# Optimization experiments

Measured on AMD Instinct MI355X. Metric: run time of the kernel, lower is better.

## Reference

```python
import jax, jax.numpy as jnp
import numpy as np

B, S, HID = 4, 1024, 768
H, D = 12, 32              # attention_head_size = (HID/H)//2
AH = H * D                 # all_head_size = 384
SCALING = D ** (-0.5)


def setup_inputs() -> dict:
    key = jax.random.key(0)
    ks = jax.random.split(key, 6)
    hidden_states = jax.random.normal(ks[0], (B, S, HID), dtype=jnp.float32)
    attention_mask = jnp.zeros((B, 1, 1, S), dtype=jnp.float32)
    init = 0.02
    Wq = jax.random.normal(ks[1], (AH, HID), dtype=jnp.float32) * init
    Wk1 = jax.random.normal(ks[2], (AH, HID), dtype=jnp.float32) * init
    Wk2 = jax.random.normal(ks[3], (AH, HID), dtype=jnp.float32) * init
    Wv = jax.random.normal(ks[4], (AH, HID), dtype=jnp.float32) * init
    bq = jnp.zeros((AH,), jnp.float32)
    bk1 = jnp.zeros((AH,), jnp.float32)
    bk2 = jnp.zeros((AH,), jnp.float32)
    bv = jnp.zeros((AH,), jnp.float32)
    pi = jnp.ones((2, H), jnp.float32) / 2.0
    return {"hidden_states": hidden_states, "attention_mask": attention_mask,
            "Wq": Wq, "bq": bq, "Wk1": Wk1, "bk1": bk1, "Wk2": Wk2, "bk2": bk2,
            "Wv": Wv, "bv": bv, "pi": pi}


def _heads(x):
    # [B,S,AH] -> [B,H,S,D]
    return x.reshape(B, S, H, D).transpose(0, 2, 1, 3)


def _sq_dist(x1, x2):
    # gpytorch Distance._sq_dist (postprocess=False): mean-adjust, then
    # ||x1||^2 + ||x2||^2 - 2 x1 x2^T, clamped at 0.
    adj = x1.mean(axis=-2, keepdims=True)
    x1 = x1 - adj
    x2 = x2 - adj
    n1 = (x1 * x1).sum(-1, keepdims=True)            # [B,H,S,1]
    n2 = (x2 * x2).sum(-1, keepdims=True)            # [B,H,S,1]
    cross = jnp.einsum('bhqd,bhkd->bhqk', x1, x2)    # [B,H,S,S]
    return jnp.maximum(n1 + jnp.swapaxes(n2, -1, -2) - 2.0 * cross, 0.0)


def reference(hidden_states, attention_mask, Wq, bq, Wk1, bk1, Wk2, bk2, Wv, bv, pi):
    q = _heads(hidden_states @ Wq.T + bq)
    k1 = _heads(hidden_states @ Wk1.T + bk1)
    k2 = _heads(hidden_states @ Wk2.T + bk2)
    v = _heads(hidden_states @ Wv.T + bv)

    d1 = -SCALING / 2.0 * _sq_dist(q, k1) + attention_mask
    d2 = -1.5 * SCALING / 2.0 * _sq_dist(q, k2) + attention_mask
    d1 = d1 - d1.max(axis=-1, keepdims=True)
    d2 = d2 - d2.max(axis=-1, keepdims=True)

    pi_c = jnp.clip(pi, 1e-6, 2.0)                   # clamp per original
    scores = (jnp.exp(d1) * pi_c[0][None, :, None, None]
              + jnp.exp(d2) * pi_c[1][None, :, None, None])
    probs = scores / (scores.sum(axis=-1, keepdims=True) + 1e-6)
    # dropout is identity in eval mode
    ctx = jnp.einsum('bhqk,bhkd->bhqd', probs, v)
    ctx = ctx.transpose(0, 2, 1, 3).reshape(B, S, AH)
    return (ctx, probs)
```

## Files before the change

### kernel.cpp

```cpp
#include <hip/hip_runtime.h>
#include <math.h>

#define BB 4
#define SS 1024
#define HH 12
#define DD 32
#define HIDDEN 768
#define AHS 384
#define RQ 8
#define HEAD_ELEMS (SS*DD)
#define CTX_ELEMS (BB*SS*AHS)

__device__ __forceinline__ float clampf(float x, float lo, float hi){ return fminf(fmaxf(x, lo), hi); }

__global__ __launch_bounds__(256)
void proj_kernel(const float* __restrict__ X,
                 const float* __restrict__ W0, const float* __restrict__ b0,
                 const float* __restrict__ W1, const float* __restrict__ b1,
                 const float* __restrict__ W2, const float* __restrict__ b2,
                 const float* __restrict__ W3, const float* __restrict__ b3,
                 float* __restrict__ qo, float* __restrict__ k1o,
                 float* __restrict__ k2o, float* __restrict__ vo)
{
    const int BM = 128, BN = 64, BK = 16;
    __shared__ float Xs[BK][BM + 4];
    __shared__ float Wsh[BK][BN + 4];
    int t  = threadIdx.x;
    int m0 = blockIdx.x * BM;
    int n0 = blockIdx.y * BN;
    int mat = n0 / AHS;
    int c0  = n0 % AHS;
    const float* W    = (mat==0) ? W0 : (mat==1) ? W1 : (mat==2) ? W2 : W3;
    const float* bias = (mat==0) ? b0 : (mat==1) ? b1 : (mat==2) ? b2 : b3;

    int tx = t & 15, ty = t >> 4;
    int lr = t >> 2;
    int lc = (t & 3) << 2;

    float acc[8][4];
    #pragma unroll
    for (int i = 0; i < 8; i++)
        #pragma unroll
        for (int j = 0; j < 4; j++) acc[i][j] = 0.f;

    float4 xa = *(const float4*)(X + (m0 + lr) * HIDDEN + lc);
    float4 xb = *(const float4*)(X + (m0 + 64 + lr) * HIDDEN + lc);
    float4 wa = *(const float4*)(W + (c0 + lr) * HIDDEN + lc);

    for (int k0 = 0; k0 < HIDDEN; k0 += BK) {
        __syncthreads();
        Xs[lc+0][lr] = xa.x; Xs[lc+1][lr] = xa.y; Xs[lc+2][lr] = xa.z; Xs[lc+3][lr] = xa.w;
        Xs[lc+0][64+lr] = xb.x; Xs[lc+1][64+lr] = xb.y; Xs[lc+2][64+lr] = xb.z; Xs[lc+3][64+lr] = xb.w;
        Wsh[lc+0][lr] = wa.x; Wsh[lc+1][lr] = wa.y; Wsh[lc+2][lr] = wa.z; Wsh[lc+3][lr] = wa.w;
        __syncthreads();
        if (k0 + BK < HIDDEN) {
            xa = *(const float4*)(X + (m0 + lr) * HIDDEN + k0 + BK + lc);
            xb = *(const float4*)(X + (m0 + 64 + lr) * HIDDEN + k0 + BK + lc);
            wa = *(const float4*)(W + (c0 + lr) * HIDDEN + k0 + BK + lc);
        }
        #pragma unroll
        for (int kk = 0; kk < BK; kk++) {
            float a[8], w4[4];
            *(float4*)&a[0] = *(const float4*)&Xs[kk][ty << 3];
            *(float4*)&a[4] = *(const float4*)&Xs[kk][(ty << 3) + 4];
            *(float4*)w4    = *(const float4*)&Wsh[kk][tx << 2];
            #pragma unroll
            for (int i = 0; i < 8; i++)
                #pragma unroll
                for (int j = 0; j < 4; j++)
                    acc[i][j] = fmaf(a[i], w4[j], acc[i][j]);
        }
    }

    int cbase = c0 + (tx << 2);
    int h  = (cbase >> 5) % HH;
    int d0 = cbase & 31;
    int d4 = d0 >> 2;
    float4 bq4 = *(const float4*)(bias + cbase);

    #pragma unroll
    for (int i = 0; i < 8; i++) {
        int row = m0 + (ty << 3) + i;
        int b_  = row >> 10;
        int s   = row & 1023;
        int bh  = b_ * HH + h;
        float4 val;
        val.x = acc[i][0] + bq4.x;
        val.y = acc[i][1] + bq4.y;
        val.z = acc[i][2] + bq4.z;
        val.w = acc[i][3] + bq4.w;
        if (mat == 0)
            *(float4*)&qo[((size_t)(bh * SS + s)) * DD + d0] = val;
        else if (mat == 1)
            *(float4*)&k1o[((size_t)(bh * 8 + d4) * SS + s) * 4] = val;
        else if (mat == 2)
            *(float4*)&k2o[((size_t)(bh * 8 + d4) * SS + s) * 4] = val;
        else
            *(float4*)&vo[((size_t)(bh * SS + s)) * DD + d0] = val;
    }
}

__global__ __launch_bounds__(256)
void norms_kernel(const float* __restrict__ k1i, const float* __restrict__ k2i,
                  float* __restrict__ n1, float* __restrict__ n2)
{
    int bh = blockIdx.y;
    int s  = blockIdx.x * 256 + threadIdx.x;
    const float* p1 = k1i + (size_t)bh * (8 * SS * 4) + s * 4;
    const float* p2 = k2i + (size_t)bh * (8 * SS * 4) + s * 4;
    float a1 = 0.f, a2 = 0.f;
    #pragma unroll
    for (int d4 = 0; d4 < 8; d4++) {
        float4 v1 = *(const float4*)&p1[(size_t)d4 * SS * 4];
        float4 v2 = *(const float4*)&p2[(size_t)d4 * SS * 4];
        a1 = fmaf(v1.x, v1.x, a1); a1 = fmaf(v1.y, v1.y, a1);
        a1 = fmaf(v1.z, v1.z, a1); a1 = fmaf(v1.w, v1.w, a1);
        a2 = fmaf(v2.x, v2.x, a2); a2 = fmaf(v2.y, v2.y, a2);
        a2 = fmaf(v2.z, v2.z, a2); a2 = fmaf(v2.w, v2.w, a2);
    }
    n1[bh * SS + s] = a1;
    n2[bh * SS + s] = a2;
}

__global__ __launch_bounds__(256, 4)
void attn_fused(const float* __restrict__ qg,  const float* __restrict__ k1i,
                const float* __restrict__ k2i,
                const float* __restrict__ n1g, const float* __restrict__ n2g,
                const float* __restrict__ maskg, const float* __restrict__ pig,
                const float* __restrict__ vg,
                float* __restrict__ probs, float* __restrict__ ctx)
{
    const float A1C = 0.08838834764831845f;
    const float A2C = 0.13258252147247767f;
    __shared__ float p_s[RQ * SS];
    __shared__ float q_s[RQ * DD];
    __shared__ float red1[4][RQ], red2[4][RQ];
    __shared__ float qn_s[RQ];

    int t    = threadIdx.x;
    int lane = t & 63, wid = t >> 6;

    int bid = blockIdx.x;
    int swz = (bid & 7) * 768 + (bid >> 3);
    int bh  = swz >> 7;
    int s0  = (swz & 127) * RQ;
    int b   = bh / HH, h = bh - b * HH;

    q_s[t] = qg[(bh * SS + s0) * DD + t];
    __syncthreads();
    if (t < RQ) {
        float a = 0.f;
        for (int d = 0; d < DD; d++) { float x = q_s[t * DD + d]; a = fmaf(x, x, a); }
        qn_s[t] = a;
    }
    __syncthreads();

    float pi0 = clampf(pig[h],      1e-6f, 2.0f);
    float pi1 = clampf(pig[HH + h], 1e-6f, 2.0f);

    float e1r[4][RQ], e2r[4][RQ];
    float pm1[RQ], pm2[RQ];
    #pragma unroll
    for (int r = 0; r < RQ; r++) { pm1[r] = -3.4e38f; pm2[r] = -3.4e38f; }

    const float* k1p = k1i + (size_t)bh * (8 * SS * 4);
    const float* k2p = k2i + (size_t)bh * (8 * SS * 4);
    const float* n1p = n1g + bh * SS;
    const float* n2p = n2g + bh * SS;
    const float* mp  = maskg + b * SS;

    #pragma unroll
    for (int j = 0; j < 4; j++) {
        int k = j * 256 + t;
        float n1k = n1p[k], n2k = n2p[k], mk = mp[k];
        float c1[RQ], c2[RQ];
        #pragma unroll
        for (int r = 0; r < RQ; r++) { c1[r] = 0.f; c2[r] = 0.f; }
        #pragma unroll
        for (int d4 = 0; d4 < 8; d4++) {
            float4 kq1 = *(const float4*)&k1p[((size_t)d4 * SS + k) * 4];
            float4 kq2 = *(const float4*)&k2p[((size_t)d4 * SS + k) * 4];
            const float* kv1 = (const float*)&kq1;
            const float* kv2 = (const float*)&kq2;
            #pragma unroll
            for (int r = 0; r < RQ; r++) {
                float qv[4];
                *(float4*)qv = *(const float4*)&q_s[r * DD + d4 * 4];
                #pragma unroll
                for (int dd = 0; dd < 4; dd++) {
                    c1[r] = fmaf(qv[dd], kv1[dd], c1[r]);
                    c2[r] = fmaf(qv[dd], kv2[dd], c2[r]);
                }
            }
        }
        #pragma unroll
        for (int r = 0; r < RQ; r++) {
            float qn  = qn_s[r];
            float d1v = fmaxf(fmaf(-2.f, c1[r], qn + n1k), 0.f);
            float d2v = fmaxf(fmaf(-2.f, c2[r], qn + n2k), 0.f);
            float ev1 = fmaf(-A1C, d1v, mk);
            float ev2 = fmaf(-A2C, d2v, mk);
            e1r[j][r] = ev1;
            e2r[j][r] = ev2;
            pm1[r] = fmaxf(pm1[r], ev1);
            pm2[r] = fmaxf(pm2[r], ev2);
        }
    }

    #pragma unroll
    for (int off = 32; off >= 1; off >>= 1)
        #pragma unroll
        for (int r = 0; r < RQ; r++) {
            pm1[r] = fmaxf(pm1[r], __shfl_xor(pm1[r], off));
            pm2[r] = fmaxf(pm2[r], __shfl_xor(pm2[r], off));
        }
    if (lane == 0) {
        #pragma unroll
        for (int r = 0; r < RQ; r++) { red1[wid][r] = pm1[r]; red2[wid][r] = pm2[r]; }
    }
    __syncthreads();
    float m1[RQ], m2[RQ];
    #pragma unroll
    for (int r = 0; r < RQ; r++) {
        m1[r] = fmaxf(fmaxf(red1[0][r], red1[1][r]), fmaxf(red1[2][r], red1[3][r]));
        m2[r] = fmaxf(fmaxf(red2[0][r], red2[1][r]), fmaxf(red2[2][r], red2[3][r]));
    }

    float ps[RQ];
    #pragma unroll
    for (int r = 0; r < RQ; r++) ps[r] = 0.f;
    #pragma unroll
    for (int j = 0; j < 4; j++)
        #pragma unroll
        for (int r = 0; r < RQ; r++) {
            float p = pi0 * __expf(e1r[j][r] - m1[r]) + pi1 * __expf(e2r[j][r] - m2[r]);
            e1r[j][r] = p;
            ps[r] += p;
        }

    #pragma unroll
    for (int off = 32; off >= 1; off >>= 1)
        #pragma unroll
        for (int r = 0; r < RQ; r++) ps[r] += __shfl_xor(ps[r], off);
    __syncthreads();
    if (lane == 0) {
        #pragma unroll
        for (int r = 0; r < RQ; r++) red1[wid][r] = ps[r];
    }
    __syncthreads();
    float inv[RQ];
    #pragma unroll
    for (int r = 0; r < RQ; r++) {
        float sum = red1[0][r] + red1[1][r] + red1[2][r] + red1[3][r];
        inv[r] = 1.0f / (sum + 1e-6f);
    }

    float* prow = probs + (size_t)(bh * SS + s0) * SS;
    #pragma unroll
    for (int j = 0; j < 4; j++) {
        int k = (j << 8) + t;
        float pv8[8];
        #pragma unroll
        for (int r = 0; r < RQ; r++) pv8[r] = e1r[j][r] * inv[r];
        #pragma unroll
        for (int r = 0; r < RQ; r++)
            __builtin_nontemporal_store(pv8[r], &prow[(size_t)r * SS + k]);
        int base = (k << 3) ^ (((k >> 5) & 3) << 3);
        *(float4*)&p_s[base]     = *(float4*)&pv8[0];
        *(float4*)&p_s[base + 4] = *(float4*)&pv8[4];
    }
    __syncthreads();

    {
        int ks = t >> 3;
        int c4 = t & 7;
        int swzc = (ks & 3) << 3;
        const float* vp = vg + bh * HEAD_ELEMS + (c4 << 2);
        float4 acc4[RQ];
        #pragma unroll
        for (int r = 0; r < RQ; r++) acc4[r] = make_float4(0.f, 0.f, 0.f, 0.f);
        #pragma unroll 4
        for (int kk = 0; kk < 32; kk++) {
            int k = (ks << 5) + kk;
            int base = (k << 3) ^ swzc;
            float pr[8];
            *(float4*)&pr[0] = *(const float4*)&p_s[base];
            *(float4*)&pr[4] = *(const float4*)&p_s[base + 4];
            float4 vv = *(const float4*)&vp[k << 5];
            #pragma unroll
            for (int r = 0; r < RQ; r++) {
                acc4[r].x = fmaf(pr[r], vv.x, acc4[r].x);
                acc4[r].y = fmaf(pr[r], vv.y, acc4[r].y);
                acc4[r].z = fmaf(pr[r], vv.z, acc4[r].z);
                acc4[r].w = fmaf(pr[r], vv.w, acc4[r].w);
            }
        }
        __syncthreads();
        #pragma unroll
        for (int r = 0; r < RQ; r++)
            *(float4*)&p_s[((ks << 8) + (r << 5) + (c4 << 2)) ^ ((ks & 3) << 3)] = acc4[r];
    }
    __syncthreads();

    {
        int rr = t >> 5, dd = t & 31;
        float o = 0.f;
        #pragma unroll
        for (int s2 = 0; s2 < 32; s2++)
            o += p_s[((s2 << 8) + (rr << 5) + dd) ^ ((s2 & 3) << 3)];
        __builtin_nontemporal_store(o, &ctx[((size_t)(b * SS + s0 + rr) * HH + h) * DD + dd]);
    }
}

extern "C" void kernel_launch(void* const* d_in, const int* in_sizes, int n_in,
                              void* d_out, int out_size, void* d_ws, size_t ws_size,
                              hipStream_t stream)
{
    const float* hs   = (const float*)d_in[0];
    const float* mask = (const float*)d_in[1];
    const float* Wq   = (const float*)d_in[2];
    const float* bq   = (const float*)d_in[3];
    const float* Wk1  = (const float*)d_in[4];
    const float* bk1  = (const float*)d_in[5];
    const float* Wk2  = (const float*)d_in[6];
    const float* bk2  = (const float*)d_in[7];
    const float* Wv   = (const float*)d_in[8];
    const float* bv   = (const float*)d_in[9];
    const float* pi   = (const float*)d_in[10];

    float* ws   = (float*)d_ws;
    float* q_ws = ws;
    float* v_ws = ws + (size_t)CTX_ELEMS * 1;
    float* k1T  = ws + (size_t)CTX_ELEMS * 2;
    float* k2T  = ws + (size_t)CTX_ELEMS * 3;
    float* n1   = ws + (size_t)CTX_ELEMS * 4;
    float* n2   = n1 + BB * HH * SS;

    float* ctx   = (float*)d_out;
    float* probs = ctx + CTX_ELEMS;

    proj_kernel<<<dim3(32, 24), 256, 0, stream>>>(hs, Wq, bq, Wk1, bk1, Wk2, bk2,
                                                  Wv, bv, q_ws, k1T, k2T, v_ws);
    norms_kernel<<<dim3(SS / 256, BB * HH), 256, 0, stream>>>(k1T, k2T, n1, n2);
    attn_fused<<<dim3(BB * HH * (SS / RQ)), 256, 0, stream>>>(q_ws, k1T, k2T,
                                                              n1, n2, mask, pi,
                                                              v_ws, probs, ctx);
}
```

Baseline: 519.9 us.

## Fuse key norms into projection, double-buffer GEMM smem, drop nontemporal stores

Removes the separate norms kernel by computing squared row norms of k1/k2 in the projection epilogue and reducing them in shared memory. It also double-buffers the projection GEMM's shared-memory tiles, so there is one barrier per K step instead of two. The nontemporal stores for probs and ctx become ordinary stores. This saves a kernel launch and a re-read of the K tensors, but changes how the large probs write interacts with the cache.

```diff
diff --git a/kernel.cpp b/kernel.cpp
--- a/kernel.cpp
+++ b/kernel.cpp
@@ -20,11 +20,12 @@
                  const float* __restrict__ W2, const float* __restrict__ b2,
                  const float* __restrict__ W3, const float* __restrict__ b3,
                  float* __restrict__ qo, float* __restrict__ k1o,
-                 float* __restrict__ k2o, float* __restrict__ vo)
+                 float* __restrict__ k2o, float* __restrict__ vo,
+                 float* __restrict__ n1, float* __restrict__ n2)
 {
     const int BM = 128, BN = 64, BK = 16;
-    __shared__ float Xs[BK][BM + 4];
-    __shared__ float Wsh[BK][BN + 4];
+    __shared__ float Xs[2][BK][BM + 4];
+    __shared__ float Wsh[2][BK][BN + 4];
     int t  = threadIdx.x;
     int m0 = blockIdx.x * BM;
     int n0 = blockIdx.y * BN;
@@ -47,13 +48,15 @@
     float4 xb = *(const float4*)(X + (m0 + 64 + lr) * HIDDEN + lc);
     float4 wa = *(const float4*)(W + (c0 + lr) * HIDDEN + lc);
 
+    Xs[0][lc+0][lr] = xa.x; Xs[0][lc+1][lr] = xa.y; Xs[0][lc+2][lr] = xa.z; Xs[0][lc+3][lr] = xa.w;
+    Xs[0][lc+0][64+lr] = xb.x; Xs[0][lc+1][64+lr] = xb.y; Xs[0][lc+2][64+lr] = xb.z; Xs[0][lc+3][64+lr] = xb.w;
+    Wsh[0][lc+0][lr] = wa.x; Wsh[0][lc+1][lr] = wa.y; Wsh[0][lc+2][lr] = wa.z; Wsh[0][lc+3][lr] = wa.w;
+    __syncthreads();
+
     for (int k0 = 0; k0 < HIDDEN; k0 += BK) {
-        __syncthreads();
-        Xs[lc+0][lr] = xa.x; Xs[lc+1][lr] = xa.y; Xs[lc+2][lr] = xa.z; Xs[lc+3][lr] = xa.w;
-        Xs[lc+0][64+lr] = xb.x; Xs[lc+1][64+lr] = xb.y; Xs[lc+2][64+lr] = xb.z; Xs[lc+3][64+lr] = xb.w;
-        Wsh[lc+0][lr] = wa.x; Wsh[lc+1][lr] = wa.y; Wsh[lc+2][lr] = wa.z; Wsh[lc+3][lr] = wa.w;
-        __syncthreads();
-        if (k0 + BK < HIDDEN) {
+        int cur = (k0 >> 4) & 1;
+        bool more = (k0 + BK < HIDDEN);
+        if (more) {
             xa = *(const float4*)(X + (m0 + lr) * HIDDEN + k0 + BK + lc);
             xb = *(const float4*)(X + (m0 + 64 + lr) * HIDDEN + k0 + BK + lc);
             wa = *(const float4*)(W + (c0 + lr) * HIDDEN + k0 + BK + lc);
@@ -61,23 +64,31 @@
         #pragma unroll
         for (int kk = 0; kk < BK; kk++) {
             float a[8], w4[4];
-            *(float4*)&a[0] = *(const float4*)&Xs[kk][ty << 3];
-            *(float4*)&a[4] = *(const float4*)&Xs[kk][(ty << 3) + 4];
-            *(float4*)w4    = *(const float4*)&Wsh[kk][tx << 2];
+            *(float4*)&a[0] = *(const float4*)&Xs[cur][kk][ty << 3];
+            *(float4*)&a[4] = *(const float4*)&Xs[cur][kk][(ty << 3) + 4];
+            *(float4*)w4    = *(const float4*)&Wsh[cur][kk][tx << 2];
             #pragma unroll
             for (int i = 0; i < 8; i++)
                 #pragma unroll
                 for (int j = 0; j < 4; j++)
                     acc[i][j] = fmaf(a[i], w4[j], acc[i][j]);
         }
+        if (more) {
+            int nxt = cur ^ 1;
+            Xs[nxt][lc+0][lr] = xa.x; Xs[nxt][lc+1][lr] = xa.y; Xs[nxt][lc+2][lr] = xa.z; Xs[nxt][lc+3][lr] = xa.w;
+            Xs[nxt][lc+0][64+lr] = xb.x; Xs[nxt][lc+1][64+lr] = xb.y; Xs[nxt][lc+2][64+lr] = xb.z; Xs[nxt][lc+3][64+lr] = xb.w;
+            Wsh[nxt][lc+0][lr] = wa.x; Wsh[nxt][lc+1][lr] = wa.y; Wsh[nxt][lc+2][lr] = wa.z; Wsh[nxt][lc+3][lr] = wa.w;
+            __syncthreads();
+        }
     }
 
     int cbase = c0 + (tx << 2);
-    int h  = (cbase >> 5) % HH;
+    int h  = cbase >> 5;
     int d0 = cbase & 31;
     int d4 = d0 >> 2;
     float4 bq4 = *(const float4*)(bias + cbase);
 
+    float psq[8];
     #pragma unroll
     for (int i = 0; i < 8; i++) {
         int row = m0 + (ty << 3) + i;
@@ -89,6 +100,7 @@
         val.y = acc[i][1] + bq4.y;
         val.z = acc[i][2] + bq4.z;
         val.w = acc[i][3] + bq4.w;
+        psq[i] = val.x*val.x + val.y*val.y + val.z*val.z + val.w*val.w;
         if (mat == 0)
             *(float4*)&qo[((size_t)(bh * SS + s)) * DD + d0] = val;
         else if (mat == 1)
@@ -98,28 +110,27 @@
         else
             *(float4*)&vo[((size_t)(bh * SS + s)) * DD + d0] = val;
     }
-}
-
-__global__ __launch_bounds__(256)
-void norms_kernel(const float* __restrict__ k1i, const float* __restrict__ k2i,
-                  float* __restrict__ n1, float* __restrict__ n2)
-{
-    int bh = blockIdx.y;
-    int s  = blockIdx.x * 256 + threadIdx.x;
-    const float* p1 = k1i + (size_t)bh * (8 * SS * 4) + s * 4;
-    const float* p2 = k2i + (size_t)bh * (8 * SS * 4) + s * 4;
-    float a1 = 0.f, a2 = 0.f;
-    #pragma unroll
-    for (int d4 = 0; d4 < 8; d4++) {
-        float4 v1 = *(const float4*)&p1[(size_t)d4 * SS * 4];
-        float4 v2 = *(const float4*)&p2[(size_t)d4 * SS * 4];
-        a1 = fmaf(v1.x, v1.x, a1); a1 = fmaf(v1.y, v1.y, a1);
-        a1 = fmaf(v1.z, v1.z, a1); a1 = fmaf(v1.w, v1.w, a1);
-        a2 = fmaf(v2.x, v2.x, a2); a2 = fmaf(v2.y, v2.y, a2);
-        a2 = fmaf(v2.z, v2.z, a2); a2 = fmaf(v2.w, v2.w, a2);
-    }
-    n1[bh * SS + s] = a1;
-    n2[bh * SS + s] = a2;
+
+    if (mat == 1 || mat == 2) {
+        float* nout = (mat == 1) ? n1 : n2;
+        float* nrm  = (float*)Xs;
+        __syncthreads();
+        int hs = tx >> 3, q8 = tx & 7;
+        #pragma unroll
+        for (int i = 0; i < 8; i++)
+            nrm[hs * 1024 + ((ty << 3) + i) * 8 + q8] = psq[i];
+        __syncthreads();
+        int hs2 = t >> 7, ri = t & 127;
+        const float* pn = &nrm[hs2 * 1024 + ri * 8];
+        float4 aq = *(const float4*)pn;
+        float4 bq = *(const float4*)(pn + 4);
+        float s8 = ((aq.x + aq.y) + (aq.z + aq.w)) + ((bq.x + bq.y) + (bq.z + bq.w));
+        int row = m0 + ri;
+        int b_  = row >> 10;
+        int s   = row & 1023;
+        int hh  = (c0 >> 5) + hs2;
+        nout[(b_ * HH + hh) * SS + s] = s8;
+    }
 }
 
 __global__ __launch_bounds__(256, 4)
@@ -263,8 +274,7 @@
         #pragma unroll
         for (int r = 0; r < RQ; r++) pv8[r] = e1r[j][r] * inv[r];
         #pragma unroll
-        for (int r = 0; r < RQ; r++)
-            __builtin_nontemporal_store(pv8[r], &prow[(size_t)r * SS + k]);
+        for (int r = 0; r < RQ; r++) prow[(size_t)r * SS + k] = pv8[r];
         int base = (k << 3) ^ (((k >> 5) & 3) << 3);
         *(float4*)&p_s[base]     = *(float4*)&pv8[0];
         *(float4*)&p_s[base + 4] = *(float4*)&pv8[4];
@@ -308,7 +318,7 @@
         #pragma unroll
         for (int s2 = 0; s2 < 32; s2++)
             o += p_s[((s2 << 8) + (rr << 5) + dd) ^ ((s2 & 3) << 3)];
-        __builtin_nontemporal_store(o, &ctx[((size_t)(b * SS + s0 + rr) * HH + h) * DD + dd]);
+        ctx[((size_t)(b * SS + s0 + rr) * HH + h) * DD + dd] = o;
     }
 }
 
@@ -340,8 +350,8 @@
     float* probs = ctx + CTX_ELEMS;
 
     proj_kernel<<<dim3(32, 24), 256, 0, stream>>>(hs, Wq, bq, Wk1, bk1, Wk2, bk2,
-                                                  Wv, bv, q_ws, k1T, k2T, v_ws);
-    norms_kernel<<<dim3(SS / 256, BB * HH), 256, 0, stream>>>(k1T, k2T, n1, n2);
+                                                  Wv, bv, q_ws, k1T, k2T, v_ws,
+                                                  n1, n2);
     attn_fused<<<dim3(BB * HH * (SS / RQ)), 256, 0, stream>>>(q_ws, k1T, k2T,
                                                               n1, n2, mask, pi,
                                                               v_ws, probs, ctx);
```

Result: no change. 519.1 us (-0.2%).
